# Optimization experiments

Hardware: AMD Instinct MI355X
Metric: run time of the kernel (lower is better)

Reference implementation:

```python
import jax, jax.numpy as jnp
import numpy as np

N = 50000       # population nodes
E = 1_600_000   # edges per edge type
F_IN = 2000     # flattened individual-graph embedding (100*20)
D = 20          # hidden channels per TransformerConv head (heads=1)
NEG_SLOPE = 0.01
BN_EPS = 1e-5


def setup_inputs() -> dict:
    key = jax.random.key(0)
    ks = jax.random.split(key, 24)
    features = jax.random.normal(ks[0], (N, F_IN), jnp.float32)
    same_index = jax.random.randint(ks[1], (2, E), 0, N, dtype=jnp.int64)
    diff_index = jax.random.randint(ks[2], (2, E), 0, N, dtype=jnp.int64)
    s0 = 1.0 / np.sqrt(F_IN)
    s1 = 1.0 / np.sqrt(D)
    # layer 0 conv params, stacked over the 2 edge types (same, diff)
    W0q = jax.random.normal(ks[3], (2, F_IN, D), jnp.float32) * s0
    W0k = jax.random.normal(ks[4], (2, F_IN, D), jnp.float32) * s0
    W0v = jax.random.normal(ks[5], (2, F_IN, D), jnp.float32) * s0
    W0s = jax.random.normal(ks[6], (2, F_IN, D), jnp.float32) * s0
    b0q = jnp.zeros((2, D)); b0k = jnp.zeros((2, D))
    b0v = jnp.zeros((2, D)); b0s = jnp.zeros((2, D))
    # layers 1..3 conv params: [layer, edge_type, D, D]
    Wq = jax.random.normal(ks[7], (3, 2, D, D), jnp.float32) * s1
    Wk = jax.random.normal(ks[8], (3, 2, D, D), jnp.float32) * s1
    Wv = jax.random.normal(ks[9], (3, 2, D, D), jnp.float32) * s1
    Ws = jax.random.normal(ks[10], (3, 2, D, D), jnp.float32) * s1
    bq = jnp.zeros((3, 2, D)); bk = jnp.zeros((3, 2, D))
    bv = jnp.zeros((3, 2, D)); bs = jnp.zeros((3, 2, D))
    w1 = jnp.full((4,), 0.8, jnp.float32)
    w2 = jnp.full((4,), 0.2, jnp.float32)
    bn_gamma = jnp.ones((4, D), jnp.float32)
    bn_beta = jnp.zeros((4, D), jnp.float32)
    Wout = jax.random.normal(ks[11], (4 * D, 2), jnp.float32) / np.sqrt(4 * D)
    bout = jnp.zeros((2,), jnp.float32)
    return dict(features=features, same_index=same_index, diff_index=diff_index,
                W0q=W0q, b0q=b0q, W0k=W0k, b0k=b0k, W0v=W0v, b0v=b0v, W0s=W0s, b0s=b0s,
                Wq=Wq, bq=bq, Wk=Wk, bk=bk, Wv=Wv, bv=bv, Ws=Ws, bs=bs,
                w1=w1, w2=w2, bn_gamma=bn_gamma, bn_beta=bn_beta, Wout=Wout, bout=bout)


def _tconv(x, edge_index, Wq, bq, Wk, bk, Wv, bv, Ws, bs):
    """PyG TransformerConv, heads=1, concat=True, root_weight=True, no edge_attr."""
    src, dst = edge_index[0], edge_index[1]
    q = x @ Wq + bq   # [N, D]
    k = x @ Wk + bk
    v = x @ Wv + bv
    logits = jnp.einsum('ed,ed->e', q[dst], k[src]) / jnp.sqrt(jnp.float32(D))  # [E]
    m = jax.ops.segment_max(logits, dst, num_segments=N)
    m = jnp.where(jnp.isfinite(m), m, jnp.float32(0.0))  # nodes with no in-edges
    e = jnp.exp(logits - m[dst])
    z = jax.ops.segment_sum(e, dst, num_segments=N)
    alpha = e / (z[dst] + 1e-16)  # PyG softmax epsilon
    agg = jax.ops.segment_sum(alpha[:, None] * v[src], dst, num_segments=N)  # [N, D]
    return agg + x @ Ws + bs  # skip (root) connection


def _bn(x, gamma, beta):
    mu = x.mean(axis=0)
    var = x.var(axis=0)
    return (x - mu) * jax.lax.rsqrt(var + BN_EPS) * gamma + beta


def reference(features, same_index, diff_index,
              W0q, b0q, W0k, b0k, W0v, b0v, W0s, b0s,
              Wq, bq, Wk, bk, Wv, bv, Ws, bs,
              w1, w2, bn_gamma, bn_beta, Wout, bout):
    x = features
    fcs = []
    for l in range(4):
        if l == 0:
            p_same = (W0q[0], b0q[0], W0k[0], b0k[0], W0v[0], b0v[0], W0s[0], b0s[0])
            p_diff = (W0q[1], b0q[1], W0k[1], b0k[1], W0v[1], b0v[1], W0s[1], b0s[1])
        else:
            i = l - 1
            p_same = (Wq[i, 0], bq[i, 0], Wk[i, 0], bk[i, 0], Wv[i, 0], bv[i, 0], Ws[i, 0], bs[i, 0])
            p_diff = (Wq[i, 1], bq[i, 1], Wk[i, 1], bk[i, 1], Wv[i, 1], bv[i, 1], Ws[i, 1], bs[i, 1])
        x1 = _tconv(x, same_index, *p_same)
        x2 = _tconv(x, diff_index, *p_diff)
        t = w1[l] + w2[l]
        x = (w1[l] / t) * x1 + (w2[l] / t) * x2
        x = _bn(x, bn_gamma[l], bn_beta[l])
        x = jax.nn.leaky_relu(x, NEG_SLOPE)
        fcs.append(x)
    fc = jnp.concatenate(fcs, axis=-1)  # [N, 80]
    return fc @ Wout + bout  # [N, 2]
```

## Files before the change

### kernel.cpp

```cpp
#include <hip/hip_runtime.h>
#include <math.h>

#define N_NODES 50000
#define E_EDGES 1600000
#define F_IN    2000
#define D       20
#define NCOL    160
#define KPAD    2016

#define INV_SQRT_D 0.22360679774997896f

typedef __bf16 bf16x8 __attribute__((ext_vector_type(8)));
typedef __bf16 bf16x4 __attribute__((ext_vector_type(4)));
typedef float  f32x4  __attribute__((ext_vector_type(4)));

__global__ void pack_kernel(
    const float* __restrict__ W0q, const float* __restrict__ W0k,
    const float* __restrict__ W0v, const float* __restrict__ W0s,
    const float* __restrict__ b0q, const float* __restrict__ b0k,
    const float* __restrict__ b0v, const float* __restrict__ b0s,
    const float* __restrict__ Wq,  const float* __restrict__ Wk,
    const float* __restrict__ Wv,  const float* __restrict__ Ws_,
    const float* __restrict__ bq,  const float* __restrict__ bk,
    const float* __restrict__ bv,  const float* __restrict__ bs_,
    __bf16* __restrict__ B0, float* __restrict__ bias0,
    float* __restrict__ WL, float* __restrict__ biasL,
    float* __restrict__ bn, int* __restrict__ deg)
{
  long idx = (long)blockIdx.x * blockDim.x + threadIdx.x;
  if (idx < (long)NCOL*KPAD) {
    int col = (int)(idx / KPAD), k = (int)(idx % KPAD);
    int et = col / 80, r = col % 80, mat = r / 20, d = r % 20;
    const float* w = (mat==0)?W0q:(mat==1)?W0s:(mat==2)?W0k:W0v;
    float v = (k < F_IN) ? w[((size_t)et*F_IN + k)*D + d] : 0.f;
    B0[idx] = (__bf16)v;
    return;
  }
  idx -= (long)NCOL*KPAD;
  if (idx < 160) {
    int col = (int)idx;
    int et = col / 80, r = col % 80, mat = r / 20, d = r % 20;
    const float* b = (mat==0)?b0q:(mat==1)?b0s:(mat==2)?b0k:b0v;
    bias0[col] = b[et*D + d];
    return;
  }
  idx -= 160;
  if (idx < 9600) {
    int l = (int)(idx / 3200), rem = (int)(idx % 3200);
    int k = rem / NCOL, col = rem % NCOL;
    int et = col / 80, r = col % 80, mat = r / 20, d = r % 20;
    const float* w = (mat==0)?Wq:(mat==1)?Ws_:(mat==2)?Wk:Wv;
    WL[idx] = w[(((size_t)l*2 + et)*D + k)*D + d];
    return;
  }
  idx -= 9600;
  if (idx < 480) {
    int l = (int)(idx / NCOL), col = (int)(idx % NCOL);
    int et = col / 80, r = col % 80, mat = r / 20, d = r % 20;
    const float* b = (mat==0)?bq:(mat==1)?bs_:(mat==2)?bk:bv;
    biasL[idx] = b[(l*2 + et)*D + d];
    return;
  }
  idx -= 480;
  if (idx < 320) { bn[idx] = 0.f; return; }
  idx -= 320;
  if (idx < 2*N_NODES) { deg[idx] = 0; return; }
}

__global__ void hist_kernel(const int* __restrict__ same, const int* __restrict__ diff,
                            int* __restrict__ deg)
{
  long i = (long)blockIdx.x * blockDim.x + threadIdx.x;
  if (i >= 2L*E_EDGES) return;
  int et = (i >= E_EDGES) ? 1 : 0;
  long e = i - (long)et*E_EDGES;
  const int* ix = et ? diff : same;
  int dst = ix[E_EDGES + e];
  atomicAdd(&deg[(size_t)et*N_NODES + dst], 1);
}

__global__ void scan_kernel(const int* __restrict__ deg,
                            int* __restrict__ rowptr0, int* __restrict__ rowptr1,
                            int* __restrict__ next0, int* __restrict__ next1)
{
  const int et = blockIdx.x;
  const int* dg = deg + (size_t)et*N_NODES;
  int* rp = et ? rowptr1 : rowptr0;
  int* np = et ? next1 : next0;
  __shared__ int part[1024];
  const int t = threadIdx.x;
  const int per = (N_NODES + 1023) / 1024;
  const int b = t * per;
  const int e = (b + per < N_NODES) ? (b + per) : N_NODES;
  int s = 0;
  for (int i = b; i < e; i++) s += dg[i];
  part[t] = s;
  __syncthreads();
  for (int o = 1; o < 1024; o <<= 1) {
    int v = (t >= o) ? part[t-o] : 0;
    __syncthreads();
    part[t] += v;
    __syncthreads();
  }
  int run = (t == 0) ? 0 : part[t-1];
  for (int i = b; i < e; i++) {
    rp[i] = run; np[i] = run;
    run += dg[i];
  }
  if (t == 0) rp[N_NODES] = part[1023];
}

#define SC_EPT 16
#define SC_CHUNK (256*SC_EPT)
__global__ void scatter_kernel(const int* __restrict__ same, const int* __restrict__ diff,
                               int* __restrict__ next0, int* __restrict__ next1,
                               int* __restrict__ adj0, int* __restrict__ adj1)
{
  const int part  = blockIdx.x & 7;
  const int chunk = blockIdx.x >> 3;
  const int lo = part * (N_NODES/8);
  const int hi = lo + (N_NODES/8);
  const long i0 = (long)chunk * SC_CHUNK + threadIdx.x;
#pragma unroll
  for (int it = 0; it < SC_EPT; ++it) {
    long i = i0 + (long)it*256;
    if (i >= 2L*E_EDGES) break;
    int et = (i >= E_EDGES) ? 1 : 0;
    long e = i - (long)et*E_EDGES;
    const int* ix = et ? diff : same;
    int dst = ix[E_EDGES + e];
    if (dst >= lo && dst < hi) {
      int src = ix[e];
      int* np  = et ? next1 : next0;
      int* adj = et ? adj1  : adj0;
      int pos = atomicAdd(&np[dst], 1);
      adj[pos] = src;
    }
  }
}

__launch_bounds__(512)
__global__ void gemm0_mfma(const float* __restrict__ A,
                           const __bf16* __restrict__ Bt,
                           const float* __restrict__ bias,
                           __bf16* __restrict__ C)
{
  __shared__ __bf16 as[128*32];
  const int t    = threadIdx.x;
  const int lane = t & 63;
  const int wid  = t >> 6;
  const int wr   = wid >> 1;
  const int wc   = wid & 1;
  const int rb0  = blockIdx.x * 128;

  const int srow = t >> 2;
  const int skc  = (t & 3) * 8;
  const int arow = rb0 + srow;
  const float* aptr = A + (size_t)arow * F_IN;

  const int lrow = lane & 15;
  const int lkb  = (lane >> 4) * 8;

  f32x4 acc[2][5];
#pragma unroll
  for (int i = 0; i < 2; i++)
#pragma unroll
    for (int j = 0; j < 5; j++) acc[i][j] = (f32x4){0.f,0.f,0.f,0.f};

  float4 p0, p1;
  auto loadA = [&](int k0) {
    int k = k0 + skc;
    if (arow < N_NODES) {
      if (k + 8 <= F_IN) {
        p0 = *(const float4*)(aptr + k);
        p1 = *(const float4*)(aptr + k + 4);
      } else {
        float tmp[8];
#pragma unroll
        for (int i = 0; i < 8; i++) tmp[i] = (k + i < F_IN) ? aptr[k + i] : 0.f;
        p0 = make_float4(tmp[0],tmp[1],tmp[2],tmp[3]);
        p1 = make_float4(tmp[4],tmp[5],tmp[6],tmp[7]);
      }
    } else {
      p0 = make_float4(0,0,0,0); p1 = p0;
    }
  };

  loadA(0);
  for (int s = 0; s < 63; s++) {
    bf16x8 h;
    h[0]=(__bf16)p0.x; h[1]=(__bf16)p0.y; h[2]=(__bf16)p0.z; h[3]=(__bf16)p0.w;
    h[4]=(__bf16)p1.x; h[5]=(__bf16)p1.y; h[6]=(__bf16)p1.z; h[7]=(__bf16)p1.w;
    *(bf16x8*)&as[srow*32 + skc] = h;
    __syncthreads();
    if (s + 1 < 63) loadA((s + 1) * 32);

    bf16x8 af[2];
#pragma unroll
    for (int rf = 0; rf < 2; rf++)
      af[rf] = *(bf16x8*)&as[(wr*32 + rf*16 + lrow)*32 + lkb];
    bf16x8 bfr[5];
#pragma unroll
    for (int cf = 0; cf < 5; cf++)
      bfr[cf] = *(const bf16x8*)(Bt + (size_t)(wc*80 + cf*16 + lrow)*KPAD + s*32 + lkb);
#pragma unroll
    for (int rf = 0; rf < 2; rf++)
#pragma unroll
      for (int cf = 0; cf < 5; cf++)
        acc[rf][cf] = __builtin_amdgcn_mfma_f32_16x16x32_bf16(af[rf], bfr[cf], acc[rf][cf], 0, 0, 0);
    __syncthreads();
  }

#pragma unroll
  for (int rf = 0; rf < 2; rf++) {
#pragma unroll
    for (int cf = 0; cf < 5; cf++) {
      int col = wc*80 + cf*16 + lrow;
      float bv = bias[col];
#pragma unroll
      for (int j = 0; j < 4; j++) {
        int r = rb0 + wr*32 + rf*16 + (lane >> 4)*4 + j;
        if (r < N_NODES) C[(size_t)r*NCOL + col] = (__bf16)(acc[rf][cf][j] + bv);
      }
    }
  }
}

__launch_bounds__(256)
__global__ void proj_small_kernel(const float* __restrict__ x, const float* __restrict__ W,
                                  const float* __restrict__ bias, __bf16* __restrict__ C)
{
  __shared__ float ws[20*160];
  __shared__ float xs[16*20];
  const int t = threadIdx.x;
  const int n0 = blockIdx.x * 16;
#pragma unroll
  for (int i = 0; i < 13; i++) {
    int idx = t + i*256;
    if (idx < 3200) ws[idx] = W[idx];
  }
#pragma unroll
  for (int i = 0; i < 2; i++) {
    int idx = t + i*256;
    if (idx < 320) {
      int nl = idx / 20, k = idx % 20;
      int n = n0 + nl;
      xs[idx] = (n < N_NODES) ? x[(size_t)n*D + k] : 0.f;
    }
  }
  __syncthreads();
#pragma unroll
  for (int i = 0; i < 10; i++) {
    int idx = t + i*256;
    int nl = idx / NCOL, col = idx % NCOL;
    int n = n0 + nl;
    if (n < N_NODES) {
      float acc = bias[col];
#pragma unroll
      for (int k = 0; k < 20; k++) acc += xs[nl*20 + k] * ws[k*NCOL + col];
      C[(size_t)n*NCOL + col] = (__bf16)acc;
    }
  }
}

__launch_bounds__(256)
__global__ void attn_kernel(const int* __restrict__ rowptr0, const int* __restrict__ adj0,
                            const int* __restrict__ rowptr1, const int* __restrict__ adj1,
                            const __bf16* __restrict__ proj,
                            float* __restrict__ out0, float* __restrict__ out1)
{
  const int et   = blockIdx.y;
  const int* rowptr = et ? rowptr1 : rowptr0;
  const int* adj    = et ? adj1 : adj0;
  float* xout       = et ? out1 : out0;

  const int t    = threadIdx.x;
  const int node = blockIdx.x*16 + (t >> 4);
  const int sl   = t & 15;
  if (node >= N_NODES) return;

  const __bf16* rq = proj + (size_t)node*NCOL + et*80;
  float qf[20];
  {
    bf16x8 q0 = *(const bf16x8*)(rq);
    bf16x8 q1 = *(const bf16x8*)(rq + 8);
    bf16x4 q2 = *(const bf16x4*)(rq + 16);
#pragma unroll
    for (int i = 0; i < 8; i++) { qf[i] = (float)q0[i]; qf[8+i] = (float)q1[i]; }
#pragma unroll
    for (int i = 0; i < 4; i++) qf[16+i] = (float)q2[i];
  }

  const int beg = rowptr[node], end = rowptr[node+1];

  float m = -INFINITY, z = 0.f;
  float S[20];
#pragma unroll
  for (int d = 0; d < 20; d++) S[d] = 0.f;

  for (int i = beg + sl; i < end; i += 16) {
    const int src = adj[i];
    const __bf16* kv = proj + (size_t)src*NCOL + et*80 + 40;
    bf16x8 c0 = *(const bf16x8*)(kv);
    bf16x8 c1 = *(const bf16x8*)(kv + 8);
    bf16x8 c2 = *(const bf16x8*)(kv + 16);
    bf16x8 c3 = *(const bf16x8*)(kv + 24);
    bf16x8 c4 = *(const bf16x8*)(kv + 32);

    float dot = 0.f;
#pragma unroll
    for (int i2 = 0; i2 < 8; i2++) dot += qf[i2]      * (float)c0[i2];
#pragma unroll
    for (int i2 = 0; i2 < 8; i2++) dot += qf[8 + i2]  * (float)c1[i2];
#pragma unroll
    for (int i2 = 0; i2 < 4; i2++) dot += qf[16 + i2] * (float)c2[i2];
    dot *= INV_SQRT_D;

    float nm = fmaxf(m, dot);
    float a  = __expf(m - nm);
    float w  = __expf(dot - nm);
    z = z*a + w;
#pragma unroll
    for (int d = 0; d < 4; d++)  S[d]      = S[d]*a      + w*(float)c2[4 + d];
#pragma unroll
    for (int d = 0; d < 8; d++)  S[4 + d]  = S[4 + d]*a  + w*(float)c3[d];
#pragma unroll
    for (int d = 0; d < 8; d++)  S[12 + d] = S[12 + d]*a + w*(float)c4[d];
    m = nm;
  }

#pragma unroll
  for (int o = 8; o >= 1; o >>= 1) {
    float m2 = __shfl_xor(m, o, 64);
    float z2 = __shfl_xor(z, o, 64);
    float nm = fmaxf(m, m2);
    float a  = __expf(fminf(m  - nm, 0.f));
    float b  = __expf(fminf(m2 - nm, 0.f));
    z = z*a + z2*b;
#pragma unroll
    for (int d = 0; d < 20; d++) {
      float s2 = __shfl_xor(S[d], o, 64);
      S[d] = S[d]*a + s2*b;
    }
    m = nm;
  }

  if (sl == 0) {
    const float inv = 1.f / (z + 1e-16f);
    const __bf16* sp = rq + 20;
    float* xo = xout + (size_t)node*D;
    float sv[20];
    {
      bf16x4 s0 = *(const bf16x4*)(sp);
      bf16x8 s1 = *(const bf16x8*)(sp + 4);
      bf16x8 s2 = *(const bf16x8*)(sp + 12);
#pragma unroll
      for (int i = 0; i < 4; i++) sv[i] = (float)s0[i];
#pragma unroll
      for (int i = 0; i < 8; i++) { sv[4+i] = (float)s1[i]; sv[12+i] = (float)s2[i]; }
    }
#pragma unroll
    for (int j = 0; j < 5; j++) {
      float4 o4;
      o4.x = S[4*j+0]*inv + sv[4*j+0];
      o4.y = S[4*j+1]*inv + sv[4*j+1];
      o4.z = S[4*j+2]*inv + sv[4*j+2];
      o4.w = S[4*j+3]*inv + sv[4*j+3];
      *(float4*)(xo + 4*j) = o4;
    }
  }
}

__global__ void combine_kernel(const float* __restrict__ A0, const float* __restrict__ A1,
                               const float* __restrict__ w1, const float* __restrict__ w2,
                               int l, float* __restrict__ xpre, float* __restrict__ bn)
{
  __shared__ float ls[40];
  const int t = threadIdx.x;
  if (t < 40) ls[t] = 0.f;
  __syncthreads();
  const int i = blockIdx.x*256 + t;
  if (i < N_NODES*D) {
    float a = w1[l], b = w2[l];
    float tt = a + b;
    float v = (a/tt)*A0[i] + (b/tt)*A1[i];
    xpre[i] = v;
    int d = i % D;
    atomicAdd(&ls[d], v);
    atomicAdd(&ls[20+d], v*v);
  }
  __syncthreads();
  if (t < 40) atomicAdd(&bn[t], ls[t]);
}

__global__ void stats_kernel(float* __restrict__ bn)
{
  int t = threadIdx.x;
  if (t < D) {
    float mu  = bn[t] * (1.f/N_NODES);
    float var = bn[20+t] * (1.f/N_NODES) - mu*mu;
    bn[40+t] = mu;
    bn[60+t] = 1.f / sqrtf(var + 1e-5f);
  }
}

__global__ void bnapply_kernel(const float* __restrict__ xpre, const float* __restrict__ bn,
                               const float* __restrict__ gamma, const float* __restrict__ beta,
                               int l, float* __restrict__ out)
{
  const int i = blockIdx.x*256 + threadIdx.x;
  if (i >= N_NODES*D) return;
  const int d = i % D;
  float v = (xpre[i] - bn[40+d]) * bn[60+d] * gamma[l*D+d] + beta[l*D+d];
  out[i] = (v > 0.f) ? v : 0.01f*v;
}

__global__ void final_kernel(const float* __restrict__ fcs, const float* __restrict__ Wout,
                             const float* __restrict__ bout, float* __restrict__ out)
{
  const int n = blockIdx.x*256 + threadIdx.x;
  if (n >= N_NODES) return;
  float a0 = bout[0], a1 = bout[1];
#pragma unroll
  for (int l = 0; l < 4; l++) {
    const float* base = fcs + (size_t)l*N_NODES*D + (size_t)n*D;
#pragma unroll
    for (int d = 0; d < D; d++) {
      float v = base[d];
      a0 += v * Wout[(l*D+d)*2 + 0];
      a1 += v * Wout[(l*D+d)*2 + 1];
    }
  }
  out[n*2+0] = a0;
  out[n*2+1] = a1;
}

extern "C" void kernel_launch(void* const* d_in, const int* in_sizes, int n_in,
                              void* d_out, int out_size, void* d_ws, size_t ws_size,
                              hipStream_t stream)
{
  const float* feat = (const float*)d_in[0];
  const int*   same = (const int*)d_in[1];
  const int*   diff = (const int*)d_in[2];
  const float* W0q = (const float*)d_in[3];
  const float* b0q = (const float*)d_in[4];
  const float* W0k = (const float*)d_in[5];
  const float* b0k = (const float*)d_in[6];
  const float* W0v = (const float*)d_in[7];
  const float* b0v = (const float*)d_in[8];
  const float* W0s = (const float*)d_in[9];
  const float* b0s = (const float*)d_in[10];
  const float* Wq  = (const float*)d_in[11];
  const float* bq  = (const float*)d_in[12];
  const float* Wk  = (const float*)d_in[13];
  const float* bk  = (const float*)d_in[14];
  const float* Wv  = (const float*)d_in[15];
  const float* bv  = (const float*)d_in[16];
  const float* Ws_ = (const float*)d_in[17];
  const float* bs_ = (const float*)d_in[18];
  const float* w1  = (const float*)d_in[19];
  const float* w2  = (const float*)d_in[20];
  const float* gamma = (const float*)d_in[21];
  const float* beta  = (const float*)d_in[22];
  const float* Wout  = (const float*)d_in[23];
  const float* bout  = (const float*)d_in[24];

  float* wsf  = (float*)d_ws;
  __bf16*  PROJ  = (__bf16*)wsf;
  float*   A0    = wsf + 4000000;
  float*   A1    = wsf + 5000000;
  float*   XPRE  = wsf + 6000000;
  float*   FCS   = wsf + 7000000;
  __bf16*  B0bf  = (__bf16*)(wsf + 11000000);
  float*   BIAS0 = wsf + 11161280;
  float*   WL    = wsf + 11161440;
  float*   BIASL = wsf + 11171040;
  float*   BN    = wsf + 11171520;
  int*     ib    = (int*)(wsf + 11171840);
  int* DEG  = ib;
  int* RP0  = ib + 100000;
  int* RP1  = ib + 150004;
  int* NX0  = ib + 200008;
  int* NX1  = ib + 250008;
  int* ADJ0 = ib + 300008;
  int* ADJ1 = ib + 1900008;

  const int packN = NCOL*KPAD + 160 + 9600 + 480 + 320 + 2*N_NODES;
  pack_kernel<<<(packN + 255)/256, 256, 0, stream>>>(
      W0q, W0k, W0v, W0s, b0q, b0k, b0v, b0s,
      Wq, Wk, Wv, Ws_, bq, bk, bv, bs_,
      B0bf, BIAS0, WL, BIASL, BN, DEG);

  hist_kernel<<<(2*E_EDGES + 255)/256, 256, 0, stream>>>(same, diff, DEG);
  scan_kernel<<<2, 1024, 0, stream>>>(DEG, RP0, RP1, NX0, NX1);
  {
    const long nchunk = (2L*E_EDGES + SC_CHUNK - 1) / SC_CHUNK;
    scatter_kernel<<<(int)(nchunk*8), 256, 0, stream>>>(same, diff, NX0, NX1, ADJ0, ADJ1);
  }

  dim3 attn_grid((N_NODES + 15)/16, 2);

  for (int l = 0; l < 4; l++) {
    if (l == 0)
      gemm0_mfma<<<(N_NODES + 127)/128, 512, 0, stream>>>(feat, B0bf, BIAS0, PROJ);
    else
      proj_small_kernel<<<(N_NODES + 15)/16, 256, 0, stream>>>(
          FCS + (size_t)(l-1)*N_NODES*D, WL + (size_t)(l-1)*3200, BIASL + (size_t)(l-1)*160, PROJ);

    attn_kernel<<<attn_grid, 256, 0, stream>>>(RP0, ADJ0, RP1, ADJ1, PROJ, A0, A1);

    combine_kernel<<<(N_NODES*D + 255)/256, 256, 0, stream>>>(A0, A1, w1, w2, l, XPRE, BN + l*80);
    stats_kernel<<<1, 64, 0, stream>>>(BN + l*80);
    bnapply_kernel<<<(N_NODES*D + 255)/256, 256, 0, stream>>>(
        XPRE, BN + l*80, gamma, beta, l, FCS + (size_t)l*N_NODES*D);
  }

  final_kernel<<<(N_NODES + 255)/256, 256, 0, stream>>>(FCS, Wout, bout, (float*)d_out);
}
```

Before: 1.173 ms.

## Fuse both edge-type attentions with combine and BN stats into one kernel

Merges the per-edge-type attention kernel, the weighted combine kernel and the stats kernel into a single kernel that handles both edge types per node, writes the combined pre-BN value and accumulates BN sums directly. The BN apply kernel now derives mean and rsqrt variance itself. The edge loop is unrolled by two so each lane keeps two gathers in flight. This removes the A0/A1 round trip through global memory and two launches per layer. In exchange the grid has half as many blocks, each doing serial work over both edge types, which costs parallelism and may raise register pressure.

New measurement: 1.099 ms. 6.3% less time.

```diff
diff --git a/kernel.cpp b/kernel.cpp
--- a/kernel.cpp
+++ b/kernel.cpp
@@ -264,144 +264,169 @@
 }
 
 __launch_bounds__(256)
-__global__ void attn_kernel(const int* __restrict__ rowptr0, const int* __restrict__ adj0,
-                            const int* __restrict__ rowptr1, const int* __restrict__ adj1,
-                            const __bf16* __restrict__ proj,
-                            float* __restrict__ out0, float* __restrict__ out1)
-{
-  const int et   = blockIdx.y;
-  const int* rowptr = et ? rowptr1 : rowptr0;
-  const int* adj    = et ? adj1 : adj0;
-  float* xout       = et ? out1 : out0;
-
-  const int t    = threadIdx.x;
+__global__ void attn_fused(const int* __restrict__ rp0, const int* __restrict__ adj0,
+                           const int* __restrict__ rp1, const int* __restrict__ adj1,
+                           const __bf16* __restrict__ proj,
+                           const float* __restrict__ w1, const float* __restrict__ w2, int l,
+                           float* __restrict__ xpre, float* __restrict__ bn)
+{
+  __shared__ float ls[40];
+  const int t  = threadIdx.x;
+  const int sl = t & 15;
   const int node = blockIdx.x*16 + (t >> 4);
-  const int sl   = t & 15;
-  if (node >= N_NODES) return;
-
-  const __bf16* rq = proj + (size_t)node*NCOL + et*80;
-  float qf[20];
-  {
-    bf16x8 q0 = *(const bf16x8*)(rq);
-    bf16x8 q1 = *(const bf16x8*)(rq + 8);
-    bf16x4 q2 = *(const bf16x4*)(rq + 16);
-#pragma unroll
-    for (int i = 0; i < 8; i++) { qf[i] = (float)q0[i]; qf[8+i] = (float)q1[i]; }
-#pragma unroll
-    for (int i = 0; i < 4; i++) qf[16+i] = (float)q2[i];
-  }
-
-  const int beg = rowptr[node], end = rowptr[node+1];
-
-  float m = -INFINITY, z = 0.f;
-  float S[20];
-#pragma unroll
-  for (int d = 0; d < 20; d++) S[d] = 0.f;
-
-  for (int i = beg + sl; i < end; i += 16) {
-    const int src = adj[i];
-    const __bf16* kv = proj + (size_t)src*NCOL + et*80 + 40;
-    bf16x8 c0 = *(const bf16x8*)(kv);
-    bf16x8 c1 = *(const bf16x8*)(kv + 8);
-    bf16x8 c2 = *(const bf16x8*)(kv + 16);
-    bf16x8 c3 = *(const bf16x8*)(kv + 24);
-    bf16x8 c4 = *(const bf16x8*)(kv + 32);
-
-    float dot = 0.f;
-#pragma unroll
-    for (int i2 = 0; i2 < 8; i2++) dot += qf[i2]      * (float)c0[i2];
-#pragma unroll
-    for (int i2 = 0; i2 < 8; i2++) dot += qf[8 + i2]  * (float)c1[i2];
-#pragma unroll
-    for (int i2 = 0; i2 < 4; i2++) dot += qf[16 + i2] * (float)c2[i2];
-    dot *= INV_SQRT_D;
-
-    float nm = fmaxf(m, dot);
-    float a  = __expf(m - nm);
-    float w  = __expf(dot - nm);
-    z = z*a + w;
-#pragma unroll
-    for (int d = 0; d < 4; d++)  S[d]      = S[d]*a      + w*(float)c2[4 + d];
-#pragma unroll
-    for (int d = 0; d < 8; d++)  S[4 + d]  = S[4 + d]*a  + w*(float)c3[d];
-#pragma unroll
-    for (int d = 0; d < 8; d++)  S[12 + d] = S[12 + d]*a + w*(float)c4[d];
-    m = nm;
-  }
-
-#pragma unroll
-  for (int o = 8; o >= 1; o >>= 1) {
-    float m2 = __shfl_xor(m, o, 64);
-    float z2 = __shfl_xor(z, o, 64);
-    float nm = fmaxf(m, m2);
-    float a  = __expf(fminf(m  - nm, 0.f));
-    float b  = __expf(fminf(m2 - nm, 0.f));
-    z = z*a + z2*b;
-#pragma unroll
-    for (int d = 0; d < 20; d++) {
-      float s2 = __shfl_xor(S[d], o, 64);
-      S[d] = S[d]*a + s2*b;
-    }
-    m = nm;
-  }
-
-  if (sl == 0) {
-    const float inv = 1.f / (z + 1e-16f);
-    const __bf16* sp = rq + 20;
-    float* xo = xout + (size_t)node*D;
-    float sv[20];
-    {
-      bf16x4 s0 = *(const bf16x4*)(sp);
-      bf16x8 s1 = *(const bf16x8*)(sp + 4);
-      bf16x8 s2 = *(const bf16x8*)(sp + 12);
-#pragma unroll
-      for (int i = 0; i < 4; i++) sv[i] = (float)s0[i];
-#pragma unroll
-      for (int i = 0; i < 8; i++) { sv[4+i] = (float)s1[i]; sv[12+i] = (float)s2[i]; }
-    }
-#pragma unroll
-    for (int j = 0; j < 5; j++) {
-      float4 o4;
-      o4.x = S[4*j+0]*inv + sv[4*j+0];
-      o4.y = S[4*j+1]*inv + sv[4*j+1];
-      o4.z = S[4*j+2]*inv + sv[4*j+2];
-      o4.w = S[4*j+3]*inv + sv[4*j+3];
-      *(float4*)(xo + 4*j) = o4;
-    }
-  }
-}
-
-__global__ void combine_kernel(const float* __restrict__ A0, const float* __restrict__ A1,
-                               const float* __restrict__ w1, const float* __restrict__ w2,
-                               int l, float* __restrict__ xpre, float* __restrict__ bn)
-{
-  __shared__ float ls[40];
-  const int t = threadIdx.x;
+  const bool valid = node < N_NODES;
   if (t < 40) ls[t] = 0.f;
   __syncthreads();
-  const int i = blockIdx.x*256 + t;
-  if (i < N_NODES*D) {
-    float a = w1[l], b = w2[l];
-    float tt = a + b;
-    float v = (a/tt)*A0[i] + (b/tt)*A1[i];
-    xpre[i] = v;
-    int d = i % D;
-    atomicAdd(&ls[d], v);
-    atomicAdd(&ls[20+d], v*v);
+
+  const float wa = w1[l], wb = w2[l];
+  const float cw[2] = { wa/(wa+wb), wb/(wa+wb) };
+  float xacc[20];
+
+#pragma unroll
+  for (int et = 0; et < 2; et++) {
+    float m = -INFINITY, z = 0.f;
+    float S[20];
+#pragma unroll
+    for (int d = 0; d < 20; d++) S[d] = 0.f;
+
+    const __bf16* rq = proj + (size_t)(valid ? node : 0)*NCOL + et*80;
+
+    if (valid) {
+      float qf[20];
+      {
+        bf16x8 q0 = *(const bf16x8*)(rq);
+        bf16x8 q1 = *(const bf16x8*)(rq + 8);
+        bf16x4 q2 = *(const bf16x4*)(rq + 16);
+#pragma unroll
+        for (int i = 0; i < 8; i++) { qf[i] = (float)q0[i]; qf[8+i] = (float)q1[i]; }
+#pragma unroll
+        for (int i = 0; i < 4; i++) qf[16+i] = (float)q2[i];
+      }
+      const int* rowptr = et ? rp1 : rp0;
+      const int* adj    = et ? adj1 : adj0;
+      const int beg = rowptr[node], end = rowptr[node+1];
+
+      int i = beg + sl;
+      for (; i + 16 < end; i += 32) {
+        const int s0 = adj[i], s1 = adj[i+16];
+        const __bf16* kva = proj + (size_t)s0*NCOL + et*80 + 40;
+        const __bf16* kvb = proj + (size_t)s1*NCOL + et*80 + 40;
+        bf16x8 a0 = *(const bf16x8*)(kva);
+        bf16x8 a1 = *(const bf16x8*)(kva + 8);
+        bf16x8 a2 = *(const bf16x8*)(kva + 16);
+        bf16x8 a3 = *(const bf16x8*)(kva + 24);
+        bf16x8 a4 = *(const bf16x8*)(kva + 32);
+        bf16x8 b0 = *(const bf16x8*)(kvb);
+        bf16x8 b1 = *(const bf16x8*)(kvb + 8);
+        bf16x8 b2 = *(const bf16x8*)(kvb + 16);
+        bf16x8 b3 = *(const bf16x8*)(kvb + 24);
+        bf16x8 b4 = *(const bf16x8*)(kvb + 32);
+
+        float d0 = 0.f, d1 = 0.f;
+#pragma unroll
+        for (int j = 0; j < 8; j++) { d0 += qf[j]*(float)a0[j];     d1 += qf[j]*(float)b0[j]; }
+#pragma unroll
+        for (int j = 0; j < 8; j++) { d0 += qf[8+j]*(float)a1[j];   d1 += qf[8+j]*(float)b1[j]; }
+#pragma unroll
+        for (int j = 0; j < 4; j++) { d0 += qf[16+j]*(float)a2[j];  d1 += qf[16+j]*(float)b2[j]; }
+        d0 *= INV_SQRT_D; d1 *= INV_SQRT_D;
+
+        float nm = fmaxf(fmaxf(m, d0), d1);
+        float a  = __expf(m - nm);
+        float w0 = __expf(d0 - nm);
+        float w1v= __expf(d1 - nm);
+        z = z*a + w0 + w1v;
+#pragma unroll
+        for (int d = 0; d < 4; d++) S[d]    = S[d]*a    + w0*(float)a2[4+d] + w1v*(float)b2[4+d];
+#pragma unroll
+        for (int d = 0; d < 8; d++) S[4+d]  = S[4+d]*a  + w0*(float)a3[d]   + w1v*(float)b3[d];
+#pragma unroll
+        for (int d = 0; d < 8; d++) S[12+d] = S[12+d]*a + w0*(float)a4[d]   + w1v*(float)b4[d];
+        m = nm;
+      }
+      for (; i < end; i += 16) {
+        const int s0 = adj[i];
+        const __bf16* kva = proj + (size_t)s0*NCOL + et*80 + 40;
+        bf16x8 a0 = *(const bf16x8*)(kva);
+        bf16x8 a1 = *(const bf16x8*)(kva + 8);
+        bf16x8 a2 = *(const bf16x8*)(kva + 16);
+        bf16x8 a3 = *(const bf16x8*)(kva + 24);
+        bf16x8 a4 = *(const bf16x8*)(kva + 32);
+        float d0 = 0.f;
+#pragma unroll
+        for (int j = 0; j < 8; j++) d0 += qf[j]*(float)a0[j];
+#pragma unroll
+        for (int j = 0; j < 8; j++) d0 += qf[8+j]*(float)a1[j];
+#pragma unroll
+        for (int j = 0; j < 4; j++) d0 += qf[16+j]*(float)a2[j];
+        d0 *= INV_SQRT_D;
+        float nm = fmaxf(m, d0);
+        float a  = __expf(m - nm);
+        float w0 = __expf(d0 - nm);
+        z = z*a + w0;
+#pragma unroll
+        for (int d = 0; d < 4; d++) S[d]    = S[d]*a    + w0*(float)a2[4+d];
+#pragma unroll
+        for (int d = 0; d < 8; d++) S[4+d]  = S[4+d]*a  + w0*(float)a3[d];
+#pragma unroll
+        for (int d = 0; d < 8; d++) S[12+d] = S[12+d]*a + w0*(float)a4[d];
+        m = nm;
+      }
+    }
+
+#pragma unroll
+    for (int o = 8; o >= 1; o >>= 1) {
+      float m2 = __shfl_xor(m, o, 64);
+      float z2 = __shfl_xor(z, o, 64);
+      float nm = fmaxf(m, m2);
+      float a  = __expf(fminf(m  - nm, 0.f));
+      float b  = __expf(fminf(m2 - nm, 0.f));
+      z = z*a + z2*b;
+#pragma unroll
+      for (int d = 0; d < 20; d++) {
+        float s2 = __shfl_xor(S[d], o, 64);
+        S[d] = S[d]*a + s2*b;
+      }
+      m = nm;
+    }
+
+    if (valid && sl == 0) {
+      const float inv = 1.f / (z + 1e-16f);
+      const __bf16* sp = rq + 20;
+      float sv[20];
+      {
+        bf16x4 s0 = *(const bf16x4*)(sp);
+        bf16x8 s1 = *(const bf16x8*)(sp + 4);
+        bf16x8 s2 = *(const bf16x8*)(sp + 12);
+#pragma unroll
+        for (int i = 0; i < 4; i++) sv[i] = (float)s0[i];
+#pragma unroll
+        for (int i = 0; i < 8; i++) { sv[4+i] = (float)s1[i]; sv[12+i] = (float)s2[i]; }
+      }
+      const float c = cw[et];
+#pragma unroll
+      for (int d = 0; d < 20; d++) {
+        float val = c * (S[d]*inv + sv[d]);
+        xacc[d] = (et == 0) ? val : (xacc[d] + val);
+      }
+    }
+  }
+
+  if (valid && sl == 0) {
+    float* xo = xpre + (size_t)node*D;
+#pragma unroll
+    for (int j = 0; j < 5; j++) {
+      float4 o4 = make_float4(xacc[4*j], xacc[4*j+1], xacc[4*j+2], xacc[4*j+3]);
+      *(float4*)(xo + 4*j) = o4;
+    }
+#pragma unroll
+    for (int d = 0; d < 20; d++) {
+      atomicAdd(&ls[d], xacc[d]);
+      atomicAdd(&ls[20+d], xacc[d]*xacc[d]);
+    }
   }
   __syncthreads();
   if (t < 40) atomicAdd(&bn[t], ls[t]);
-}
-
-__global__ void stats_kernel(float* __restrict__ bn)
-{
-  int t = threadIdx.x;
-  if (t < D) {
-    float mu  = bn[t] * (1.f/N_NODES);
-    float var = bn[20+t] * (1.f/N_NODES) - mu*mu;
-    bn[40+t] = mu;
-    bn[60+t] = 1.f / sqrtf(var + 1e-5f);
-  }
 }
 
 __global__ void bnapply_kernel(const float* __restrict__ xpre, const float* __restrict__ bn,
@@ -411,7 +436,10 @@
   const int i = blockIdx.x*256 + threadIdx.x;
   if (i >= N_NODES*D) return;
   const int d = i % D;
-  float v = (xpre[i] - bn[40+d]) * bn[60+d] * gamma[l*D+d] + beta[l*D+d];
+  const float mu  = bn[d] * (1.f/N_NODES);
+  const float var = bn[20+d] * (1.f/N_NODES) - mu*mu;
+  const float rs  = rsqrtf(var + 1e-5f);
+  float v = (xpre[i] - mu) * rs * gamma[l*D+d] + beta[l*D+d];
   out[i] = (v > 0.f) ? v : 0.01f*v;
 }
 
@@ -467,8 +495,6 @@
 
   float* wsf  = (float*)d_ws;
   __bf16*  PROJ  = (__bf16*)wsf;
-  float*   A0    = wsf + 4000000;
-  float*   A1    = wsf + 5000000;
   float*   XPRE  = wsf + 6000000;
   float*   FCS   = wsf + 7000000;
   __bf16*  B0bf  = (__bf16*)(wsf + 11000000);
@@ -498,8 +524,6 @@
     scatter_kernel<<<(int)(nchunk*8), 256, 0, stream>>>(same, diff, NX0, NX1, ADJ0, ADJ1);
   }
 
-  dim3 attn_grid((N_NODES + 15)/16, 2);
-
   for (int l = 0; l < 4; l++) {
     if (l == 0)
       gemm0_mfma<<<(N_NODES + 127)/128, 512, 0, stream>>>(feat, B0bf, BIAS0, PROJ);
@@ -507,10 +531,9 @@
       proj_small_kernel<<<(N_NODES + 15)/16, 256, 0, stream>>>(
           FCS + (size_t)(l-1)*N_NODES*D, WL + (size_t)(l-1)*3200, BIASL + (size_t)(l-1)*160, PROJ);
 
-    attn_kernel<<<attn_grid, 256, 0, stream>>>(RP0, ADJ0, RP1, ADJ1, PROJ, A0, A1);
-
-    combine_kernel<<<(N_NODES*D + 255)/256, 256, 0, stream>>>(A0, A1, w1, w2, l, XPRE, BN + l*80);
-    stats_kernel<<<1, 64, 0, stream>>>(BN + l*80);
+    attn_fused<<<(N_NODES + 15)/16, 256, 0, stream>>>(
+        RP0, ADJ0, RP1, ADJ1, PROJ, w1, w2, l, XPRE, BN + l*80);
+
     bnapply_kernel<<<(N_NODES*D + 255)/256, 256, 0, stream>>>(
         XPRE, BN + l*80, gamma, beta, l, FCS + (size_t)l*N_NODES*D);
   }
```
